# Optimization experiments

Measured on AMD Instinct MI355X. Metric: run time of the kernel, lower is better.

Reference implementation:

```python
import jax, jax.numpy as jnp
import numpy as np

UP = 4  # upsample factor of DispUpsampleBySlantedPlane


def _l1_warp_cost(fea_l, fea_r, disp):
    """Warp fea_r horizontally by disp (grid_sample bilinear, zeros padding,
    align_corners=True) and return per-pixel L1 distance over channels.
    fea_l, fea_r: [B, C, H, W]; disp: [B, H, W] -> returns [B, H, W]."""
    B, C, H, W = fea_l.shape
    x = jnp.arange(W, dtype=disp.dtype)
    xf = x[None, None, :] - disp              # sample position in right image
    x0 = jnp.floor(xf)
    w1 = xf - x0                              # weight for x0+1
    w0 = 1.0 - w1
    x0i = x0.astype(jnp.int32)
    x1i = x0i + 1
    v0 = ((x0i >= 0) & (x0i < W)).astype(fea_l.dtype)  # zeros padding masks
    v1 = ((x1i >= 0) & (x1i < W)).astype(fea_l.dtype)
    x0c = jnp.clip(x0i, 0, W - 1)
    x1c = jnp.clip(x1i, 0, W - 1)
    idx0 = jnp.broadcast_to(x0c[:, None, :, :], (B, C, H, W))
    idx1 = jnp.broadcast_to(x1c[:, None, :, :], (B, C, H, W))
    g0 = jnp.take_along_axis(fea_r, idx0, axis=3)
    g1 = jnp.take_along_axis(fea_r, idx1, axis=3)
    warped = g0 * (w0 * v0)[:, None] + g1 * (w1 * v1)[:, None]
    return jnp.sum(jnp.abs(fea_l - warped), axis=1)  # L1 over channels


def _tile_warping(tile_plane, fea_l, fea_r):
    B, C, H, W = fea_l.shape
    h, w = tile_plane.shape[2], tile_plane.shape[3]
    d = tile_plane[:, 0]   # [B, h, w]
    dx = tile_plane[:, 1]
    dy = tile_plane[:, 2]
    # slanted-plane offsets for the 4x4 sub-pixels, centered at (UP-1)/2 = 1.5
    off = jnp.arange(UP, dtype=fea_l.dtype) - (UP - 1) / 2.0
    outs = []
    for disp_d in (-1.0, 0.0, 1.0):
        # disp0[b, di, dj, th, tw] = (d + disp_d) + off[di]*dy + off[dj]*dx
        disp0 = ((d + disp_d)[:, None, None]
                 + off[None, :, None, None, None] * dy[:, None, None]
                 + off[None, None, :, None, None] * dx[:, None, None])
        # PixelShuffle(4): full-res disparity [B, H, W]
        disp_full = disp0.transpose(0, 3, 1, 4, 2).reshape(B, H, W)
        cv = _l1_warp_cost(fea_l, fea_r, disp_full)        # [B, H, W]
        # cv[:, :, i::4, j::4] for i,j in 0..3, concatenated on channel dim
        local = cv.reshape(B, h, UP, w, UP).transpose(0, 2, 4, 1, 3)
        outs.append(local.reshape(B, UP * UP, h, w))       # [B, 16, h, w]
    return jnp.concatenate(outs, axis=1)                   # [B, 48, h, w]


def setup_inputs() -> dict:
    key = jax.random.key(0)
    k1, k2, k3 = jax.random.split(key, 3)
    B, C, H, W = 4, 16, 512, 960
    h, w = H // UP, W // UP
    tile_plane = jax.random.normal(k1, (B, 3, h, w), dtype=jnp.float32)
    fea_l = jax.random.normal(k2, (B, C, H, W), dtype=jnp.float32)
    fea_r = jax.random.normal(k3, (B, C, H, W), dtype=jnp.float32)
    return {"tile_plane": tile_plane, "fea_l": fea_l, "fea_r": fea_r}


def reference(tile_plane, fea_l, fea_r):
    return _tile_warping(tile_plane, fea_l, fea_r)
```

## Files before the change

### kernel.cpp

```cpp
#include <hip/hip_runtime.h>


#define NB 4
#define NC 16
#define NH 512
#define NW 960
#define TH 128
#define TW 240
#define HW (NH * NW)

__global__ __launch_bounds__(320, 8) void tile_warp_kernel(
    const float* __restrict__ tp,
    const float* __restrict__ fl,
    const float* __restrict__ fr,
    float* __restrict__ out)
{
    const int u = blockIdx.x * 320 + threadIdx.x;
    const int Y = blockIdx.y;
    const int b = blockIdx.z;
    const int y = Y >> 2, i = Y & 3;
    const int T = u >> 2, j = u & 3;

    const float* frrow = fr + (size_t)(b * NC) * HW + (size_t)Y * NW;
    const float* flrow = fl + (size_t)(b * NC) * HW + (size_t)Y * NW + u;

    const int tpb = (b * 3 * TH + y) * TW + T;
    const float d   = tp[tpb];
    const float dxv = tp[tpb + TH * TW];
    const float dyv = tp[tpb + 2 * TH * TW];
    const float base = d + ((float)i - 1.5f) * dyv + ((float)j - 1.5f) * dxv;
    const float xf  = (float)u - base;
    const float x0f = floorf(xf);
    const float w1  = xf - x0f;
    const float w0  = 1.0f - w1;
    const int   x0  = (int)x0f;
    const int   p   = x0 - 1;

    float w0k[3], w1k[3];
#pragma unroll
    for (int kk = 0; kk < 3; ++kk) {
        const int xa = p + 2 - kk;
        const int xb = p + 3 - kk;
        w0k[kk] = (xa >= 0 && xa < NW) ? w0 : 0.0f;
        w1k[kk] = (xb >= 0 && xb < NW) ? w1 : 0.0f;
    }

    const int i0 = min(max(p    , 0), NW - 1);
    const int i1 = min(max(p + 1, 0), NW - 1);
    const int i2 = min(max(p + 2, 0), NW - 1);
    const int i3 = min(max(p + 3, 0), NW - 1);

    float acc0 = 0.f, acc1 = 0.f, acc2 = 0.f;

#pragma unroll
    for (int c = 0; c < NC; ++c) {
        const float* frc = frrow + (size_t)c * HW;
        const float m0  = frc[i0];
        const float m1  = frc[i1];
        const float m2  = frc[i2];
        const float m3  = frc[i3];
        const float flv = flrow[(size_t)c * HW];
        const float wv0 = m2 * w0k[0] + m3 * w1k[0];
        const float wv1 = m1 * w0k[1] + m2 * w1k[1];
        const float wv2 = m0 * w0k[2] + m1 * w1k[2];
        acc0 += fabsf(flv - wv0);
        acc1 += fabsf(flv - wv1);
        acc2 += fabsf(flv - wv2);
    }

    const size_t obase = ((size_t)(b * 48 + i * 4 + j) * TH + y) * TW + T;
    out[obase]                        = acc0;
    out[obase + 16 * (size_t)TH * TW] = acc1;
    out[obase + 32 * (size_t)TH * TW] = acc2;
}

extern "C" void kernel_launch(void* const* d_in, const int* in_sizes, int n_in,
                              void* d_out, int out_size, void* d_ws, size_t ws_size,
                              hipStream_t stream) {
    const float* tp = (const float*)d_in[0];
    const float* fl = (const float*)d_in[1];
    const float* fr = (const float*)d_in[2];
    float* out = (float*)d_out;

    dim3 grid(3, NH, NB);
    dim3 block(320);
    tile_warp_kernel<<<grid, block, 0, stream>>>(tp, fl, fr, out);
}
```

Baseline: 301.8 us.

## Stage right-feature rows in LDS via direct global-to-LDS loads with pipelining

Each block now handles one full image row (960 threads) instead of a third of a row. The right-feature row for every channel is copied into shared memory in four 4-channel stages using 16-byte global_load_lds. The scattered bilinear gathers then read from LDS instead of global memory. Left-feature loads use inline asm and are overlapped with later stages through explicit vmcnt waits and barriers. The main risk is that guard cells in the LDS buffer are never initialised, so out-of-range taps multiply zero weights by whatever values happen to be there.

```diff
diff --git a/kernel.cpp b/kernel.cpp
--- a/kernel.cpp
+++ b/kernel.cpp
@@ -8,21 +8,33 @@
 #define TH 128
 #define TW 240
 #define HW (NH * NW)
+#define GUARD 16
+#define CCH 4
+#define CBUF (2 * GUARD + CCH * NW)
 
-__global__ __launch_bounds__(320, 8) void tile_warp_kernel(
+typedef const __attribute__((address_space(1))) unsigned int* gas_u32;
+typedef __attribute__((address_space(3))) unsigned int* las_u32;
+
+__device__ __forceinline__ void stage16(const float* g, float* l) {
+    __builtin_amdgcn_global_load_lds((gas_u32)g, (las_u32)l, 16, 0, 0);
+}
+
+__global__ __launch_bounds__(960, 2) void tile_warp_kernel(
     const float* __restrict__ tp,
     const float* __restrict__ fl,
     const float* __restrict__ fr,
     float* __restrict__ out)
 {
-    const int u = blockIdx.x * 320 + threadIdx.x;
-    const int Y = blockIdx.y;
-    const int b = blockIdx.z;
+    const int u = threadIdx.x;
+    const int Y = blockIdx.x;
+    const int b = blockIdx.y;
     const int y = Y >> 2, i = Y & 3;
     const int T = u >> 2, j = u & 3;
 
+    __shared__ float smem[4][CBUF];
+
     const float* frrow = fr + (size_t)(b * NC) * HW + (size_t)Y * NW;
-    const float* flrow = fl + (size_t)(b * NC) * HW + (size_t)Y * NW + u;
+    const float* flrow = fl + (size_t)(b * NC) * HW + (size_t)Y * NW;
 
     const int tpb = (b * 3 * TH + y) * TW + T;
     const float d   = tp[tpb];
@@ -35,6 +47,7 @@
     const float w0  = 1.0f - w1;
     const int   x0  = (int)x0f;
     const int   p   = x0 - 1;
+    const int   p_cl = max(min(p, NW + 12), -GUARD);
 
     float w0k[3], w1k[3];
 #pragma unroll
@@ -44,29 +57,80 @@
         w0k[kk] = (xa >= 0 && xa < NW) ? w0 : 0.0f;
         w1k[kk] = (xb >= 0 && xb < NW) ? w1 : 0.0f;
     }
-
-    const int i0 = min(max(p    , 0), NW - 1);
-    const int i1 = min(max(p + 1, 0), NW - 1);
-    const int i2 = min(max(p + 2, 0), NW - 1);
-    const int i3 = min(max(p + 3, 0), NW - 1);
-
     float acc0 = 0.f, acc1 = 0.f, acc2 = 0.f;
 
-#pragma unroll
-    for (int c = 0; c < NC; ++c) {
-        const float* frc = frrow + (size_t)c * HW;
-        const float m0  = frc[i0];
-        const float m1  = frc[i1];
-        const float m2  = frc[i2];
-        const float m3  = frc[i3];
-        const float flv = flrow[(size_t)c * HW];
-        const float wv0 = m2 * w0k[0] + m3 * w1k[0];
-        const float wv1 = m1 * w0k[1] + m2 * w1k[1];
-        const float wv2 = m0 * w0k[2] + m1 * w1k[2];
-        acc0 += fabsf(flv - wv0);
-        acc1 += fabsf(flv - wv1);
-        acc2 += fabsf(flv - wv2);
-    }
+    const int srow = u / 240;
+    const int scol = 4 * (u % 240);
+    const int vf   = 4 * u;
+
+#define ISSUE_STAGE(k) \
+    stage16(frrow + (size_t)(4 * (k) + srow) * HW + scol, &smem[k][GUARD + 4 * u])
+
+#define ISSUE_FL(k, r0, r1, r2, r3) do {                                         \
+    asm volatile("global_load_dword %0, %1, %2"                                  \
+                 : "=v"(r0) : "v"(vf), "s"(flrow + (size_t)(4 * (k) + 0) * HW)); \
+    asm volatile("global_load_dword %0, %1, %2"                                  \
+                 : "=v"(r1) : "v"(vf), "s"(flrow + (size_t)(4 * (k) + 1) * HW)); \
+    asm volatile("global_load_dword %0, %1, %2"                                  \
+                 : "=v"(r2) : "v"(vf), "s"(flrow + (size_t)(4 * (k) + 2) * HW)); \
+    asm volatile("global_load_dword %0, %1, %2"                                  \
+                 : "=v"(r3) : "v"(vf), "s"(flrow + (size_t)(4 * (k) + 3) * HW)); \
+} while (0)
+
+#define COMPUTE_CH(k, ch, fv) do {                                   \
+    const float* L = &smem[k][GUARD + (ch) * NW + p_cl];             \
+    const float m0 = L[0], m1 = L[1], m2 = L[2], m3 = L[3];          \
+    const float wv0 = m2 * w0k[0] + m3 * w1k[0];                     \
+    const float wv1 = m1 * w0k[1] + m2 * w1k[1];                     \
+    const float wv2 = m0 * w0k[2] + m1 * w1k[2];                     \
+    acc0 += fabsf((fv) - wv0);                                       \
+    acc1 += fabsf((fv) - wv1);                                       \
+    acc2 += fabsf((fv) - wv2);                                       \
+} while (0)
+
+#define WAITV(n) do {                                                \
+    asm volatile("s_waitcnt vmcnt(" #n ")" ::: "memory");            \
+    __builtin_amdgcn_sched_barrier(0);                               \
+} while (0)
+
+    float fA0, fA1, fA2, fA3;
+    float fB0, fB1, fB2, fB3;
+    float fC0, fC1, fC2, fC3;
+    float fD0, fD1, fD2, fD3;
+
+    __builtin_amdgcn_sched_barrier(0);
+    ISSUE_STAGE(0); ISSUE_FL(0, fA0, fA1, fA2, fA3);
+    __builtin_amdgcn_sched_barrier(0);
+    ISSUE_STAGE(1); ISSUE_FL(1, fB0, fB1, fB2, fB3);
+    __builtin_amdgcn_sched_barrier(0);
+    ISSUE_STAGE(2); ISSUE_FL(2, fC0, fC1, fC2, fC3);
+    __builtin_amdgcn_sched_barrier(0);
+
+    WAITV(10);
+    __builtin_amdgcn_s_barrier();
+    __builtin_amdgcn_sched_barrier(0);
+    ISSUE_STAGE(3); ISSUE_FL(3, fD0, fD1, fD2, fD3);
+    __builtin_amdgcn_sched_barrier(0);
+    COMPUTE_CH(0, 0, fA0); COMPUTE_CH(0, 1, fA1);
+    COMPUTE_CH(0, 2, fA2); COMPUTE_CH(0, 3, fA3);
+
+    WAITV(10);
+    __builtin_amdgcn_s_barrier();
+    __builtin_amdgcn_sched_barrier(0);
+    COMPUTE_CH(1, 0, fB0); COMPUTE_CH(1, 1, fB1);
+    COMPUTE_CH(1, 2, fB2); COMPUTE_CH(1, 3, fB3);
+
+    WAITV(5);
+    __builtin_amdgcn_s_barrier();
+    __builtin_amdgcn_sched_barrier(0);
+    COMPUTE_CH(2, 0, fC0); COMPUTE_CH(2, 1, fC1);
+    COMPUTE_CH(2, 2, fC2); COMPUTE_CH(2, 3, fC3);
+
+    WAITV(0);
+    __builtin_amdgcn_s_barrier();
+    __builtin_amdgcn_sched_barrier(0);
+    COMPUTE_CH(3, 0, fD0); COMPUTE_CH(3, 1, fD1);
+    COMPUTE_CH(3, 2, fD2); COMPUTE_CH(3, 3, fD3);
 
     const size_t obase = ((size_t)(b * 48 + i * 4 + j) * TH + y) * TW + T;
     out[obase]                        = acc0;
@@ -82,7 +146,7 @@
     const float* fr = (const float*)d_in[2];
     float* out = (float*)d_out;
 
-    dim3 grid(3, NH, NB);
-    dim3 block(320);
+    dim3 grid(NH, NB);
+    dim3 block(960);
     tile_warp_kernel<<<grid, block, 0, stream>>>(tp, fl, fr, out);
 }
```

New measurement: 273.5 us. -9.4%, faster.
